# Kernel tuning notes

Hardware: AMD Instinct MI355X
Metric: run time of the kernel (lower is better)

The kernel has to match this reference:

```python
import jax, jax.numpy as jnp
import numpy as np

EPS = 1e-12  # matches torch F.normalize eps


def _l2_normalize(x):
    n = jnp.linalg.norm(x, axis=-1, keepdims=True)
    return x / jnp.maximum(n, EPS)


def setup_inputs() -> dict:
    key = jax.random.key(0)
    k1, k2, k3 = jax.random.split(key, 3)
    N, E, D = 100000, 1200000, 64
    feat = jax.random.normal(k1, (N, D), dtype=jnp.float32)
    beta = jnp.ones((1,), dtype=jnp.float32)
    src = jax.random.randint(k2, (E,), 0, N, dtype=jnp.int32)
    dst = jax.random.randint(k3, (E,), 0, N, dtype=jnp.int32)
    return {"feat": feat, "beta": beta, "src": src, "dst": dst}


def reference(feat, beta, src, dst):
    N = feat.shape[0]
    # cosine similarity on each edge (AGNN att_type)
    nh = _l2_normalize(feat)                                  # [N, D]
    e = beta[0] * jnp.sum(nh[src] * nh[dst], axis=-1)         # [E]
    # edge softmax over incoming edges of each destination node
    emax = jax.ops.segment_max(e, dst, num_segments=N)        # [N]
    emax = jnp.where(jnp.isfinite(emax), emax, 0.0)           # isolated nodes
    p = jnp.exp(e - emax[dst])                                # [E]
    psum = jax.ops.segment_sum(p, dst, num_segments=N)        # [N]
    p = p / jnp.maximum(psum[dst], EPS)                       # [E]
    # weighted scatter-sum aggregation: h_i' = sum_j p_ij * h_j
    msg = feat[src] * p[:, None]                              # [E, D]
    out = jax.ops.segment_sum(msg, dst, num_segments=N)       # [N, D]
    return out
```

## Files before the change

kernel.cpp:

```cpp
#include <hip/hip_runtime.h>
#include <hip/hip_fp16.h>

#define D 64
#define EPS 1e-12f
#define NPB 512
#define NPB_SHIFT 9
#define NB 256
#define CAP 8192
#define CAP_SHIFT 13
#define EPB 4096
#define SRC_BITS 17

typedef _Float16 hv2 __attribute__((ext_vector_type(2)));

__device__ inline unsigned bc_u(__half2 h) { return __builtin_bit_cast(unsigned, h); }
__device__ inline __half2  bc_h(unsigned u) { return __builtin_bit_cast(__half2, u); }

__device__ inline float fdot2f(unsigned a, unsigned b, float c) {
#if defined(__has_builtin) && __has_builtin(__builtin_amdgcn_fdot2)
    return __builtin_amdgcn_fdot2(__builtin_bit_cast(hv2, a),
                                  __builtin_bit_cast(hv2, b), c, false);
#else
    __half2 ah = bc_h(a), bh = bc_h(b);
    return c + __low2float(ah) * __low2float(bh)
             + __high2float(ah) * __high2float(bh);
#endif
}

__global__ __launch_bounds__(1024) void scatter_kernel(
        const int* __restrict__ src,
        const int* __restrict__ dst,
        int* __restrict__ bincursor,
        unsigned* __restrict__ pairs, int E) {
    __shared__ int hist[NB], offs[NB], cursor[NB], gbase[NB], tmp[NB];
    __shared__ int dstbuf[EPB];
    __shared__ unsigned buf[EPB];
    __shared__ unsigned char binof[EPB];

    int tid  = threadIdx.x;
    int base = blockIdx.x * EPB;
    int cnt  = min(EPB, E - base);

    if (tid < NB) hist[tid] = 0;
    __syncthreads();
    for (int i = tid; i < cnt; i += 1024) {
        int dd = dst[base + i];
        dstbuf[i] = dd;
        atomicAdd(&hist[dd >> NPB_SHIFT], 1);
    }
    __syncthreads();
    int v = 0;
    if (tid < NB) { v = hist[tid]; tmp[tid] = v; }
    __syncthreads();
    #pragma unroll
    for (int off = 1; off < NB; off <<= 1) {
        int t = 0;
        if (tid < NB && tid >= off) t = tmp[tid - off];
        __syncthreads();
        if (tid < NB) tmp[tid] += t;
        __syncthreads();
    }
    if (tid < NB) {
        int e = tmp[tid] - v;
        offs[tid] = e; cursor[tid] = e;
        if (v > 0)
            gbase[tid] = (tid << CAP_SHIFT) + atomicAdd(&bincursor[tid], v);
    }
    __syncthreads();
    for (int i = tid; i < cnt; i += 1024) {
        int s = src[base + i], dd = dstbuf[i];
        int b = dd >> NPB_SHIFT;
        int l = atomicAdd(&cursor[b], 1);
        buf[l]   = ((unsigned)(dd & (NPB - 1)) << SRC_BITS) | (unsigned)s;
        binof[l] = (unsigned char)b;
    }
    __syncthreads();
    for (int i = tid; i < cnt; i += 1024) {
        int b = binof[i];
        pairs[gbase[b] + (i - offs[b])] = buf[i];
    }
}

__global__ __launch_bounds__(1024) void csr_nh_kernel(
        const unsigned* __restrict__ pairs,
        const int* __restrict__ bincursor,
        int* __restrict__ rowbeg,
        int* __restrict__ rowend,
        int* __restrict__ esrc,
        const float4* __restrict__ feat4,
        float* __restrict__ norms,
        uint2* __restrict__ nh2,
        int N, int nbins) {
    __shared__ unsigned buf[CAP];
    __shared__ int hist[NPB], cursor[NPB], tmp[NPB];

    if ((int)blockIdx.x >= nbins) {
        int gid = (blockIdx.x - nbins) * 1024 + threadIdx.x;
        int row = gid >> 4;
        int lg  = gid & 15;
        if (row >= N) return;
        float4 v = feat4[row * 16 + lg];
        float ss = v.x * v.x + v.y * v.y + v.z * v.z + v.w * v.w;
        #pragma unroll
        for (int off = 1; off < 16; off <<= 1) ss += __shfl_xor(ss, off, 64);
        float nrm = fmaxf(sqrtf(ss), EPS);
        float inv = 1.0f / nrm;
        if (lg == 0) norms[row] = nrm;
        uint2 p;
        p.x = bc_u(__floats2half2_rn(v.x * inv, v.y * inv));
        p.y = bc_u(__floats2half2_rn(v.z * inv, v.w * inv));
        nh2[row * 16 + lg] = p;
        return;
    }

    int b    = blockIdx.x;
    int tid  = threadIdx.x;
    int base = b << CAP_SHIFT;
    int cnt  = bincursor[b];
    int node0 = b << NPB_SHIFT;

    if (tid < NPB) hist[tid] = 0;
    __syncthreads();
    for (int i = tid; i < cnt; i += 1024) {
        unsigned p = pairs[base + i];
        buf[i] = p;
        atomicAdd(&hist[p >> SRC_BITS], 1);
    }
    __syncthreads();
    int v = 0;
    if (tid < NPB) { v = hist[tid]; tmp[tid] = v; }
    __syncthreads();
    #pragma unroll
    for (int off = 1; off < NPB; off <<= 1) {
        int t = 0;
        if (tid < NPB && tid >= off) t = tmp[tid - off];
        __syncthreads();
        if (tid < NPB) tmp[tid] += t;
        __syncthreads();
    }
    if (tid < NPB) {
        int excl = tmp[tid] - v;
        cursor[tid] = excl;
        int node = node0 + tid;
        if (node < N) { rowbeg[node] = base + excl; rowend[node] = base + excl + v; }
    }
    __syncthreads();
    for (int i = tid; i < cnt; i += 1024) {
        unsigned p = buf[i];
        int pos = atomicAdd(&cursor[p >> SRC_BITS], 1);
        esrc[base + pos] = (int)(p & ((1u << SRC_BITS) - 1));
    }
}

__global__ __launch_bounds__(256) void gather_kernel(const uint4* __restrict__ nh4,
                                                     const float* __restrict__ norms,
                                                     const float* __restrict__ beta_p,
                                                     const int* __restrict__ rowbeg,
                                                     const int* __restrict__ rowend,
                                                     const int* __restrict__ esrc,
                                                     float4* __restrict__ out4, int N) {
    int t    = blockIdx.x * 256 + threadIdx.x;
    int lane = threadIdx.x & 63;
    int g    = lane >> 3;
    int lg   = lane & 7;
    int d    = (t >> 6) * 8 + g;
    if (d >= N) return;

    int j   = rowbeg[d];
    int end = rowend[d];
    float beta = beta_p[0];

    uint4 fdp = nh4[(size_t)d * 8 + lg];

    __half2 acc0 = __float2half2_rn(0.f), acc1 = acc0, acc2 = acc0, acc3 = acc0;
    float ps = 0.f;

    for (; j < end; j += 4) {
        bool v1 = (j + 1 < end), v2 = (j + 2 < end), v3 = (j + 3 < end);
        int s0 = esrc[j];
        int s1 = v1 ? esrc[j + 1] : s0;
        int s2 = v2 ? esrc[j + 2] : s0;
        int s3 = v3 ? esrc[j + 3] : s0;
        uint4 p0 = nh4[(size_t)s0 * 8 + lg];
        uint4 p1 = nh4[(size_t)s1 * 8 + lg];
        uint4 p2 = nh4[(size_t)s2 * 8 + lg];
        uint4 p3 = nh4[(size_t)s3 * 8 + lg];
        float n0 = norms[s0], n1 = norms[s1], n2 = norms[s2], n3 = norms[s3];
        float d0 = fdot2f(p0.x, fdp.x, 0.f), d1 = fdot2f(p1.x, fdp.x, 0.f);
        float d2 = fdot2f(p2.x, fdp.x, 0.f), d3 = fdot2f(p3.x, fdp.x, 0.f);
        d0 = fdot2f(p0.y, fdp.y, d0); d1 = fdot2f(p1.y, fdp.y, d1);
        d2 = fdot2f(p2.y, fdp.y, d2); d3 = fdot2f(p3.y, fdp.y, d3);
        d0 = fdot2f(p0.z, fdp.z, d0); d1 = fdot2f(p1.z, fdp.z, d1);
        d2 = fdot2f(p2.z, fdp.z, d2); d3 = fdot2f(p3.z, fdp.z, d3);
        d0 = fdot2f(p0.w, fdp.w, d0); d1 = fdot2f(p1.w, fdp.w, d1);
        d2 = fdot2f(p2.w, fdp.w, d2); d3 = fdot2f(p3.w, fdp.w, d3);
        #pragma unroll
        for (int off = 1; off < 8; off <<= 1) {
            d0 += __shfl_xor(d0, off, 64);
            d1 += __shfl_xor(d1, off, 64);
            d2 += __shfl_xor(d2, off, 64);
            d3 += __shfl_xor(d3, off, 64);
        }
        float w0 = __expf(beta * d0);
        float w1 = v1 ? __expf(beta * d1) : 0.f;
        float w2 = v2 ? __expf(beta * d2) : 0.f;
        float w3 = v3 ? __expf(beta * d3) : 0.f;
        __half2 q0 = __float2half2_rn(w0 * n0);
        __half2 q1 = __float2half2_rn(w1 * n1);
        __half2 q2 = __float2half2_rn(w2 * n2);
        __half2 q3 = __float2half2_rn(w3 * n3);
        acc0 = __hfma2(q0, bc_h(p0.x), acc0); acc0 = __hfma2(q1, bc_h(p1.x), acc0);
        acc0 = __hfma2(q2, bc_h(p2.x), acc0); acc0 = __hfma2(q3, bc_h(p3.x), acc0);
        acc1 = __hfma2(q0, bc_h(p0.y), acc1); acc1 = __hfma2(q1, bc_h(p1.y), acc1);
        acc1 = __hfma2(q2, bc_h(p2.y), acc1); acc1 = __hfma2(q3, bc_h(p3.y), acc1);
        acc2 = __hfma2(q0, bc_h(p0.z), acc2); acc2 = __hfma2(q1, bc_h(p1.z), acc2);
        acc2 = __hfma2(q2, bc_h(p2.z), acc2); acc2 = __hfma2(q3, bc_h(p3.z), acc2);
        acc3 = __hfma2(q0, bc_h(p0.w), acc3); acc3 = __hfma2(q1, bc_h(p1.w), acc3);
        acc3 = __hfma2(q2, bc_h(p2.w), acc3); acc3 = __hfma2(q3, bc_h(p3.w), acc3);
        ps += w0 + w1 + w2 + w3;
    }

    float r = 1.0f / fmaxf(ps, EPS);
    float4 o0 = {__low2float(acc0) * r, __high2float(acc0) * r,
                 __low2float(acc1) * r, __high2float(acc1) * r};
    float4 o1 = {__low2float(acc2) * r, __high2float(acc2) * r,
                 __low2float(acc3) * r, __high2float(acc3) * r};
    out4[(size_t)d * 16 + lg * 2]     = o0;
    out4[(size_t)d * 16 + lg * 2 + 1] = o1;
}

extern "C" void kernel_launch(void* const* d_in, const int* in_sizes, int n_in,
                              void* d_out, int out_size, void* d_ws, size_t ws_size,
                              hipStream_t stream) {
    const float* feat = (const float*)d_in[0];
    const float* beta = (const float*)d_in[1];
    const int*   src  = (const int*)d_in[2];
    const int*   dst  = (const int*)d_in[3];

    int N = in_sizes[0] / D;
    int E = in_sizes[2];
    int nbins = (N + NPB - 1) / NPB;

    unsigned* pairs     = (unsigned*)d_ws;
    int*      esrc      = (int*)(pairs + (size_t)nbins * CAP);
    unsigned* nhraw     = (unsigned*)(esrc + (size_t)nbins * CAP);
    float*    norms     = (float*)(nhraw + (size_t)N * 32);
    int*      bincursor = (int*)(norms + N);
    int*      rowbeg    = bincursor + NB;
    int*      rowend    = rowbeg + N;

    hipMemsetAsync(bincursor, 0, NB * sizeof(int), stream);

    int BS = (E + EPB - 1) / EPB;
    int BI = (N * 16 + 1023) / 1024;
    scatter_kernel<<<BS, 1024, 0, stream>>>(src, dst, bincursor, pairs, E);
    csr_nh_kernel<<<nbins + BI, 1024, 0, stream>>>(
        pairs, bincursor, rowbeg, rowend, esrc,
        (const float4*)feat, norms, (uint2*)nhraw, N, nbins);
    gather_kernel<<<(N + 31) / 32, 256, 0, stream>>>(
        (const uint4*)nhraw, norms, beta, rowbeg, rowend, esrc,
        (float4*)d_out, N);
}
```

Baseline: 134.8 us.

## Keep bucketing records in registers using atomic ranks instead of LDS buffers

Both binning kernels now keep each thread's records in registers. Each record's slot within its bucket comes from the return value of the shared histogram atomicAdd, which replaces the separate second counting-sort pass through shared memory. The scatter kernel drops its block-wide prefix scan entirely, and the CSR kernel replaces its barrier-heavy Hillis-Steele scan with a wave-shuffle scan. This cuts LDS traffic and barriers, lowers shared-memory use so more blocks can be resident, and runs scatter at 512 threads. In exchange, output writes within a bucket are less coalesced, and the CSR kernel relies on a bin holding at most 8192 entries (8 per thread).

```diff
diff --git a/kernel.cpp b/kernel.cpp
--- a/kernel.cpp
+++ b/kernel.cpp
@@ -27,58 +27,42 @@
 #endif
 }
 
-__global__ __launch_bounds__(1024) void scatter_kernel(
+__global__ __launch_bounds__(512) void scatter_kernel(
         const int* __restrict__ src,
         const int* __restrict__ dst,
         int* __restrict__ bincursor,
         unsigned* __restrict__ pairs, int E) {
-    __shared__ int hist[NB], offs[NB], cursor[NB], gbase[NB], tmp[NB];
-    __shared__ int dstbuf[EPB];
-    __shared__ unsigned buf[EPB];
-    __shared__ unsigned char binof[EPB];
-
+    __shared__ int hist[NB], gbase[NB];
     int tid  = threadIdx.x;
     int base = blockIdx.x * EPB;
     int cnt  = min(EPB, E - base);
 
     if (tid < NB) hist[tid] = 0;
     __syncthreads();
-    for (int i = tid; i < cnt; i += 1024) {
-        int dd = dst[base + i];
-        dstbuf[i] = dd;
-        atomicAdd(&hist[dd >> NPB_SHIFT], 1);
-    }
-    __syncthreads();
-    int v = 0;
-    if (tid < NB) { v = hist[tid]; tmp[tid] = v; }
-    __syncthreads();
-    #pragma unroll
-    for (int off = 1; off < NB; off <<= 1) {
-        int t = 0;
-        if (tid < NB && tid >= off) t = tmp[tid - off];
-        __syncthreads();
-        if (tid < NB) tmp[tid] += t;
-        __syncthreads();
-    }
+
+    unsigned rec[8];
+    int      meta[8];
+    #pragma unroll
+    for (int k = 0; k < 8; k++) {
+        int i = tid + (k << 9);
+        if (i < cnt) {
+            int s = src[base + i], dd = dst[base + i];
+            int b = dd >> NPB_SHIFT;
+            rec[k]  = ((unsigned)(dd & (NPB - 1)) << SRC_BITS) | (unsigned)s;
+            meta[k] = (b << 16) | atomicAdd(&hist[b], 1);
+        } else meta[k] = -1;
+    }
+    __syncthreads();
     if (tid < NB) {
-        int e = tmp[tid] - v;
-        offs[tid] = e; cursor[tid] = e;
+        int v = hist[tid];
         if (v > 0)
             gbase[tid] = (tid << CAP_SHIFT) + atomicAdd(&bincursor[tid], v);
     }
     __syncthreads();
-    for (int i = tid; i < cnt; i += 1024) {
-        int s = src[base + i], dd = dstbuf[i];
-        int b = dd >> NPB_SHIFT;
-        int l = atomicAdd(&cursor[b], 1);
-        buf[l]   = ((unsigned)(dd & (NPB - 1)) << SRC_BITS) | (unsigned)s;
-        binof[l] = (unsigned char)b;
-    }
-    __syncthreads();
-    for (int i = tid; i < cnt; i += 1024) {
-        int b = binof[i];
-        pairs[gbase[b] + (i - offs[b])] = buf[i];
-    }
+    #pragma unroll
+    for (int k = 0; k < 8; k++)
+        if (meta[k] >= 0)
+            pairs[gbase[meta[k] >> 16] + (meta[k] & 0xffff)] = rec[k];
 }
 
 __global__ __launch_bounds__(1024) void csr_nh_kernel(
@@ -91,8 +75,8 @@
         float* __restrict__ norms,
         uint2* __restrict__ nh2,
         int N, int nbins) {
-    __shared__ unsigned buf[CAP];
-    __shared__ int hist[NPB], cursor[NPB], tmp[NPB];
+    __shared__ int hist[NPB], offs[NPB];
+    __shared__ int wsum[8];
 
     if ((int)blockIdx.x >= nbins) {
         int gid = (blockIdx.x - nbins) * 1024 + threadIdx.x;
@@ -121,35 +105,44 @@
 
     if (tid < NPB) hist[tid] = 0;
     __syncthreads();
-    for (int i = tid; i < cnt; i += 1024) {
-        unsigned p = pairs[base + i];
-        buf[i] = p;
-        atomicAdd(&hist[p >> SRC_BITS], 1);
-    }
-    __syncthreads();
-    int v = 0;
-    if (tid < NPB) { v = hist[tid]; tmp[tid] = v; }
-    __syncthreads();
-    #pragma unroll
-    for (int off = 1; off < NPB; off <<= 1) {
-        int t = 0;
-        if (tid < NPB && tid >= off) t = tmp[tid - off];
-        __syncthreads();
-        if (tid < NPB) tmp[tid] += t;
-        __syncthreads();
-    }
+
+    unsigned rec[8];
+    int      meta[8];
+    #pragma unroll
+    for (int k = 0; k < 8; k++) {
+        int i = tid + (k << 10);
+        if (i < cnt) {
+            unsigned p = pairs[base + i];
+            int ln  = (int)(p >> SRC_BITS);
+            rec[k]  = p & ((1u << SRC_BITS) - 1);
+            meta[k] = (ln << 16) | atomicAdd(&hist[ln], 1);
+        } else meta[k] = -1;
+    }
+    __syncthreads();
+    int lane = tid & 63, w = tid >> 6;
+    int v = 0, x = 0;
+    if (tid < NPB) { v = hist[tid]; x = v; }
+    #pragma unroll
+    for (int off = 1; off < 64; off <<= 1) {
+        int t = __shfl_up(x, off, 64);
+        if (lane >= off) x += t;
+    }
+    if (tid < NPB && lane == 63) wsum[w] = x;
+    __syncthreads();
     if (tid < NPB) {
-        int excl = tmp[tid] - v;
-        cursor[tid] = excl;
+        int add = 0;
+        #pragma unroll
+        for (int ww = 0; ww < 8; ww++) add += (ww < w) ? wsum[ww] : 0;
+        int excl = x + add - v;
+        offs[tid] = excl;
         int node = node0 + tid;
         if (node < N) { rowbeg[node] = base + excl; rowend[node] = base + excl + v; }
     }
     __syncthreads();
-    for (int i = tid; i < cnt; i += 1024) {
-        unsigned p = buf[i];
-        int pos = atomicAdd(&cursor[p >> SRC_BITS], 1);
-        esrc[base + pos] = (int)(p & ((1u << SRC_BITS) - 1));
-    }
+    #pragma unroll
+    for (int k = 0; k < 8; k++)
+        if (meta[k] >= 0)
+            esrc[base + offs[meta[k] >> 16] + (meta[k] & 0xffff)] = (int)rec[k];
 }
 
 __global__ __launch_bounds__(256) void gather_kernel(const uint4* __restrict__ nh4,
@@ -253,7 +246,7 @@
 
     int BS = (E + EPB - 1) / EPB;
     int BI = (N * 16 + 1023) / 1024;
-    scatter_kernel<<<BS, 1024, 0, stream>>>(src, dst, bincursor, pairs, E);
+    scatter_kernel<<<BS, 512, 0, stream>>>(src, dst, bincursor, pairs, E);
     csr_nh_kernel<<<nbins + BI, 1024, 0, stream>>>(
         pairs, bincursor, rowbeg, rowend, esrc,
         (const float4*)feat, norms, (uint2*)nhraw, N, nbins);
```

Measured after the change: 137.5 us. No clear change (+2.0%).
